# Optimization experiments

Hardware: AMD Instinct MI355X
Metric: run time of the kernel (lower is better)

## Reference

```python
import jax, jax.numpy as jnp
import numpy as np

OUT, IN = 14336, 4096          # Llama FFN up-projection
N = OUT * IN                   # total quantized elements
NB = N // 64                   # NF4 blocks (blocksize 64)
NG = N // 256                  # double-quant groups (group size 256)
B = 32                         # batch rows


def setup_inputs() -> dict:
    key = jax.random.key(0)
    ks = jax.random.split(key, 7)
    x = jax.random.normal(ks[0], (B, IN), dtype=jnp.float16)
    # packed bytes: two 4-bit nibbles per byte (values 0..255)
    packed = jax.random.randint(ks[1], (N // 2,), 0, 256, dtype=jnp.int32)
    absmax = jax.random.uniform(ks[2], (NB,), dtype=jnp.float32)                     # per-block absmax
    code = jax.random.uniform(ks[3], (NB,), jnp.float32, minval=0.5, maxval=1.5)     # per-block code scale
    offset = jax.random.uniform(ks[4], (NB,), jnp.float32, minval=0.0, maxval=8.0)   # per-block offset
    g_absmax = jax.random.uniform(ks[5], (NG,), jnp.float32, minval=0.5, maxval=1.5) # nested (state2) absmax
    g_code = jax.random.uniform(ks[6], (NG,), jnp.float32, minval=0.5, maxval=1.5)   # nested (state2) code
    return {"x": x, "packed": packed, "absmax": absmax, "code": code,
            "offset": offset, "g_absmax": g_absmax, "g_code": g_code}


def _dequantize_nf4(packed, absmax, code, offset, g_absmax, g_code):
    # Unpack nibbles: even element = low nibble (byte & 15), odd = high nibble (byte >> 4)
    low = packed & 15
    high = packed >> 4
    nib = jnp.stack([low, high], axis=-1).reshape(-1).astype(jnp.float32)  # [N]
    # Nested (double) dequantization scales, matching the Triton kernel:
    # combined_scale = (absmax / code) * (g_absmax / g_code)
    block_scale = absmax / code                      # [NB]
    group_scale = g_absmax / g_code                  # [NG]
    cs_block = block_scale * jnp.repeat(group_scale, 64 * 4 // 64)  # each group spans 4 blocks -> [NB]
    cs = jnp.repeat(cs_block, 64)                    # per-element combined scale [N]
    off = jnp.repeat(offset, 64)                     # per-element offset [N]
    # dequantized = nibble * cs - offset * cs (as written in the kernel), stored as fp16
    deq = (nib * cs - off * cs).astype(jnp.float16)
    return deq.reshape(OUT, IN)


def reference(x, packed, absmax, code, offset, g_absmax, g_code):
    W = _dequantize_nf4(packed, absmax, code, offset, g_absmax, g_code)  # [OUT, IN] fp16
    return x @ W.T                                                        # [B, OUT] fp16
```

## Files before the change

kernel.cpp:

```cpp
#include <hip/hip_runtime.h>
#include <hip/hip_bf16.h>


#define OUT_D 14336
#define IN_D  4096
#define B_D   32
#define KC    256
#define OTILE 32
#define CHUNKS (IN_D / KC)
#define LSTRIDE 264

typedef __attribute__((ext_vector_type(4))) float f32x4;
typedef __attribute__((ext_vector_type(4))) int   i32x4;
typedef __bf16 bf16x8 __attribute__((ext_vector_type(8)));
typedef __bf16 bf16x4 __attribute__((ext_vector_type(4)));
using u16 = unsigned short;

__global__ __launch_bounds__(256) void nf4_linear_kernel(
    const float* __restrict__ x,
    const int*  __restrict__ packed,
    const float* __restrict__ absmax,
    const float* __restrict__ code,
    const float* __restrict__ offset,
    const float* __restrict__ g_absmax,
    const float* __restrict__ g_code,
    float* __restrict__ out)
{
    __shared__ u16 wlds[2][OTILE * LSTRIDE];
    __shared__ u16 xlds[2][B_D * LSTRIDE];

    const int t      = threadIdx.x;
    const int o_base = blockIdx.x * OTILE;

    const int wrow = t >> 3;
    const int wseg = t & 7;
    const int o    = o_base + wrow;

    const int wave   = t >> 6;
    const int lane   = t & 63;
    const int m_base = (wave & 1) * 16;
    const int n_base = (wave >> 1) * 16;
    const int frow   = lane & 15;
    const int kk     = (lane >> 4) * 8;

    const int* pbase = packed + o * (IN_D / 2) + wseg * 16;

    f32x4 acc = {0.f, 0.f, 0.f, 0.f};

    i32x4 pkA[4], pkB[4];
    f32x4 pxA[8], pxB[8];
    float amA, cdA, ofA, gaA, gcA;
    float amB, cdB, ofB, gaB, gcB;

#define LOADPK(DST, KCI) { \
    const i32x4* ps = reinterpret_cast<const i32x4*>(pbase + (KCI) * (KC / 2)); \
    DST[0] = ps[0]; DST[1] = ps[1]; DST[2] = ps[2]; DST[3] = ps[3]; }

#define LOADPX(DST, KCI) { \
    const float* xb = x + (KCI) * KC; \
    _Pragma("unroll") \
    for (int j = 0; j < 8; ++j) { \
        int li = t + j * 256; \
        DST[j] = *reinterpret_cast<const f32x4*>(xb + (li >> 6) * IN_D + (li & 63) * 4); } }

#define LOADSC(AM, CD, OF, GA, GC, KCI) { \
    int bidx = o * 64 + (KCI) * 4 + (wseg >> 1); \
    int gidx = o * 16 + (KCI); \
    AM = absmax[bidx]; CD = code[bidx]; OF = offset[bidx]; \
    GA = g_absmax[gidx]; GC = g_code[gidx]; }

#define BODY(PK, PX, AM, CD, OF, GA, GC, PKN, PXN, AMN, CDN, OFN, GAN, GCN, KCI) { \
     \
    if ((KCI) + 1 < CHUNKS) { \
        LOADPK(PKN, (KCI) + 1); \
        LOADPX(PXN, (KCI) + 1); \
        LOADSC(AMN, CDN, OFN, GAN, GCN, (KCI) + 1); \
    } \
     \
    { \
        const float cs  = (AM / CD) * (GA / GC); \
        const float noc = -OF * cs; \
        u16* wdst = &wlds[p][wrow * LSTRIDE + wseg * 32]; \
        _Pragma("unroll") \
        for (int j = 0; j < 4; ++j) { \
            bf16x8 r; \
            _Pragma("unroll") \
            for (int wi = 0; wi < 4; ++wi) { \
                int w = PK[j][wi]; \
                r[wi * 2]     = (__bf16)fmaf((float)(w & 15),        cs, noc); \
                r[wi * 2 + 1] = (__bf16)fmaf((float)((w >> 4) & 15), cs, noc); \
            } \
            *reinterpret_cast<bf16x8*>(wdst + j * 8) = r; \
        } \
    } \
     \
    { \
        _Pragma("unroll") \
        for (int j = 0; j < 8; ++j) { \
            int li = t + j * 256; \
            bf16x4 h; \
            h[0] = (__bf16)PX[j][0]; h[1] = (__bf16)PX[j][1]; \
            h[2] = (__bf16)PX[j][2]; h[3] = (__bf16)PX[j][3]; \
            *reinterpret_cast<bf16x4*>(&xlds[p][(li >> 6) * LSTRIDE + (li & 63) * 4]) = h; \
        } \
    } \
    __syncthreads(); \
     \
    { \
        const u16* xp = &xlds[p][(m_base + frow) * LSTRIDE + kk]; \
        const u16* wp = &wlds[p][(n_base + frow) * LSTRIDE + kk]; \
        _Pragma("unroll") \
        for (int ks = 0; ks < KC / 32; ++ks) { \
            bf16x8 a = *reinterpret_cast<const bf16x8*>(xp + ks * 32); \
            bf16x8 b = *reinterpret_cast<const bf16x8*>(wp + ks * 32); \
            acc = __builtin_amdgcn_mfma_f32_16x16x32_bf16(a, b, acc, 0, 0, 0); \
        } \
    } \
    p ^= 1; }

    LOADPK(pkA, 0);
    LOADPX(pxA, 0);
    LOADSC(amA, cdA, ofA, gaA, gcA, 0);

    int p = 0;
    for (int ic = 0; ic < CHUNKS; ic += 2) {
        BODY(pkA, pxA, amA, cdA, ofA, gaA, gcA,
             pkB, pxB, amB, cdB, ofB, gaB, gcB, ic);
        BODY(pkB, pxB, amB, cdB, ofB, gaB, gcB,
             pkA, pxA, amA, cdA, ofA, gaA, gcA, ic + 1);
    }

    const int oc = o_base + n_base + frow;
    const int r0 = m_base + (lane >> 4) * 4;
    #pragma unroll
    for (int i = 0; i < 4; ++i) {
        out[(r0 + i) * OUT_D + oc] = acc[i];
    }
}

extern "C" void kernel_launch(void* const* d_in, const int* in_sizes, int n_in,
                              void* d_out, int out_size, void* d_ws, size_t ws_size,
                              hipStream_t stream) {
    const void* px = nullptr;
    const void* ppk = nullptr;
    const void* trio[3] = {nullptr, nullptr, nullptr};
    const void* pair[2] = {nullptr, nullptr};
    int ntrio = 0, npair = 0;
    const int SZ_X   = B_D * IN_D;
    const int SZ_PK  = OUT_D * (IN_D / 2);
    const int SZ_NB  = OUT_D * (IN_D / 64);
    const int SZ_NG  = OUT_D * (IN_D / 256);
    for (int i = 0; i < n_in; ++i) {
        int s = in_sizes[i];
        if (s == SZ_X) px = d_in[i];
        else if (s == SZ_PK) ppk = d_in[i];
        else if (s == SZ_NB) { if (ntrio < 3) trio[ntrio++] = d_in[i]; }
        else if (s == SZ_NG) { if (npair < 2) pair[npair++] = d_in[i]; }
    }
    if (!px || !ppk || ntrio != 3 || npair != 2) {
        px = d_in[0]; ppk = d_in[1];
        trio[0] = d_in[2]; trio[1] = d_in[3]; trio[2] = d_in[4];
        pair[0] = d_in[5]; pair[1] = d_in[6];
    }

    nf4_linear_kernel<<<dim3(OUT_D / OTILE), dim3(256), 0, stream>>>(
        (const float*)px, (const int*)ppk,
        (const float*)trio[0], (const float*)trio[1], (const float*)trio[2],
        (const float*)pair[0], (const float*)pair[1],
        (float*)d_out);
}
```

Measured before the change: 42.31 us.

## Split K across two blocks with atomic accumulation and smaller chunks

Adds a split-K dimension (KSPLIT=2) to the grid so each block handles half of the input dimension, halving chunk size to 128 and accumulating partial outputs with atomicAdd after a memset of the output. The 448-block grid becomes 896 blocks, which is meant to fill more of the GPU's compute units and hide memory latency. Per-block scales are now precomputed at load time, and launch bounds request 4 blocks per CU. The cost is an extra memset launch, atomic traffic on the output, and more loop iterations with barriers.

```diff
diff --git a/kernel.cpp b/kernel.cpp
--- a/kernel.cpp
+++ b/kernel.cpp
@@ -5,10 +5,11 @@
 #define OUT_D 14336
 #define IN_D  4096
 #define B_D   32
-#define KC    256
+#define KC    128
 #define OTILE 32
-#define CHUNKS (IN_D / KC)
-#define LSTRIDE 264
+#define KSPLIT 2
+#define CHUNKS (IN_D / KC / KSPLIT)
+#define LSTRIDE 136
 
 typedef __attribute__((ext_vector_type(4))) float f32x4;
 typedef __attribute__((ext_vector_type(4))) int   i32x4;
@@ -16,7 +17,7 @@
 typedef __bf16 bf16x4 __attribute__((ext_vector_type(4)));
 using u16 = unsigned short;
 
-__global__ __launch_bounds__(256) void nf4_linear_kernel(
+__global__ __launch_bounds__(256, 4) void nf4_kernel(
     const float* __restrict__ x,
     const int*  __restrict__ packed,
     const float* __restrict__ absmax,
@@ -31,6 +32,7 @@
 
     const int t      = threadIdx.x;
     const int o_base = blockIdx.x * OTILE;
+    const int kz     = blockIdx.y;
 
     const int wrow = t >> 3;
     const int wseg = t & 7;
@@ -43,69 +45,67 @@
     const int frow   = lane & 15;
     const int kk     = (lane >> 4) * 8;
 
-    const int* pbase = packed + o * (IN_D / 2) + wseg * 16;
+    const int*   pbase = packed + o * (IN_D / 2) + kz * (IN_D / 4);
+    const float* xbase = x + kz * (IN_D / 2);
+    const int    sb    = o * 64 + kz * 32;
+    const int    gb    = o * 16;
 
     f32x4 acc = {0.f, 0.f, 0.f, 0.f};
 
-    i32x4 pkA[4], pkB[4];
-    f32x4 pxA[8], pxB[8];
-    float amA, cdA, ofA, gaA, gcA;
-    float amB, cdB, ofB, gaB, gcB;
+    i32x4 pkA[2], pkB[2];
+    f32x4 pxA[4], pxB[4];
+    float csA[2], nocA[2], csB[2], nocB[2];
 
-#define LOADPK(DST, KCI) { \
-    const i32x4* ps = reinterpret_cast<const i32x4*>(pbase + (KCI) * (KC / 2)); \
-    DST[0] = ps[0]; DST[1] = ps[1]; DST[2] = ps[2]; DST[3] = ps[3]; }
+#define LOADPK(DST, C) { \
+    DST[0] = *reinterpret_cast<const i32x4*>(pbase + (C) * 64 + wseg * 4); \
+    DST[1] = *reinterpret_cast<const i32x4*>(pbase + (C) * 64 + 32 + wseg * 4); }
 
-#define LOADPX(DST, KCI) { \
-    const float* xb = x + (KCI) * KC; \
+#define LOADPX(DST, C) { \
     _Pragma("unroll") \
-    for (int j = 0; j < 8; ++j) { \
-        int li = t + j * 256; \
-        DST[j] = *reinterpret_cast<const f32x4*>(xb + (li >> 6) * IN_D + (li & 63) * 4); } }
+    for (int j2 = 0; j2 < 4; ++j2) { \
+        int li = t + j2 * 256; \
+        DST[j2] = *reinterpret_cast<const f32x4*>( \
+            xbase + (li >> 5) * IN_D + (C) * KC + (li & 31) * 4); } }
 
-#define LOADSC(AM, CD, OF, GA, GC, KCI) { \
-    int bidx = o * 64 + (KCI) * 4 + (wseg >> 1); \
-    int gidx = o * 16 + (KCI); \
-    AM = absmax[bidx]; CD = code[bidx]; OF = offset[bidx]; \
-    GA = g_absmax[gidx]; GC = g_code[gidx]; }
+#define LOADSC(CS, NOC, C) { \
+    _Pragma("unroll") \
+    for (int j = 0; j < 2; ++j) { \
+        int blk = kz * 32 + (C) * 2 + j;        \
+        int bi  = sb + (C) * 2 + j; \
+        int gi  = gb + (blk >> 2); \
+        float am = absmax[bi], cd = code[bi], of = offset[bi]; \
+        float ga = g_absmax[gi], gc = g_code[gi]; \
+        CS[j]  = (am * ga) / (cd * gc); \
+        NOC[j] = -of * CS[j]; } }
 
-#define BODY(PK, PX, AM, CD, OF, GA, GC, PKN, PXN, AMN, CDN, OFN, GAN, GCN, KCI) { \
-     \
-    if ((KCI) + 1 < CHUNKS) { \
-        LOADPK(PKN, (KCI) + 1); \
-        LOADPX(PXN, (KCI) + 1); \
-        LOADSC(AMN, CDN, OFN, GAN, GCN, (KCI) + 1); \
+#define BODY(PK, PX, CS, NOC, PKN, PXN, CSN, NOCN, C) { \
+    if ((C) + 1 < CHUNKS) { \
+        LOADPK(PKN, (C) + 1) \
+        LOADPX(PXN, (C) + 1) \
+        LOADSC(CSN, NOCN, (C) + 1) \
     } \
      \
-    { \
-        const float cs  = (AM / CD) * (GA / GC); \
-        const float noc = -OF * cs; \
-        u16* wdst = &wlds[p][wrow * LSTRIDE + wseg * 32]; \
+    _Pragma("unroll") \
+    for (int j = 0; j < 2; ++j) { \
+        bf16x8 r; \
         _Pragma("unroll") \
-        for (int j = 0; j < 4; ++j) { \
-            bf16x8 r; \
-            _Pragma("unroll") \
-            for (int wi = 0; wi < 4; ++wi) { \
-                int w = PK[j][wi]; \
-                r[wi * 2]     = (__bf16)fmaf((float)(w & 15),        cs, noc); \
-                r[wi * 2 + 1] = (__bf16)fmaf((float)((w >> 4) & 15), cs, noc); \
-            } \
-            *reinterpret_cast<bf16x8*>(wdst + j * 8) = r; \
+        for (int q = 0; q < 4; ++q) { \
+            int w = PK[j][q]; \
+            r[2 * q]     = (__bf16)fmaf((float)(w & 15),        CS[j], NOC[j]); \
+            r[2 * q + 1] = (__bf16)fmaf((float)((w >> 4) & 15), CS[j], NOC[j]); \
         } \
+        *reinterpret_cast<bf16x8*>(&wlds[p][wrow * LSTRIDE + (j * 8 + wseg) * 8]) = r; \
     } \
      \
-    { \
-        _Pragma("unroll") \
-        for (int j = 0; j < 8; ++j) { \
-            int li = t + j * 256; \
-            bf16x4 h; \
-            h[0] = (__bf16)PX[j][0]; h[1] = (__bf16)PX[j][1]; \
-            h[2] = (__bf16)PX[j][2]; h[3] = (__bf16)PX[j][3]; \
-            *reinterpret_cast<bf16x4*>(&xlds[p][(li >> 6) * LSTRIDE + (li & 63) * 4]) = h; \
-        } \
+    _Pragma("unroll") \
+    for (int j2 = 0; j2 < 4; ++j2) { \
+        int li = t + j2 * 256; \
+        bf16x4 h; \
+        h[0] = (__bf16)PX[j2][0]; h[1] = (__bf16)PX[j2][1]; \
+        h[2] = (__bf16)PX[j2][2]; h[3] = (__bf16)PX[j2][3]; \
+        *reinterpret_cast<bf16x4*>(&xlds[p][(li >> 5) * LSTRIDE + (li & 31) * 4]) = h; \
     } \
     __syncthreads(); \
-     \
     { \
         const u16* xp = &xlds[p][(m_base + frow) * LSTRIDE + kk]; \
         const u16* wp = &wlds[p][(n_base + frow) * LSTRIDE + kk]; \
@@ -118,24 +118,26 @@
     } \
     p ^= 1; }
 
-    LOADPK(pkA, 0);
-    LOADPX(pxA, 0);
-    LOADSC(amA, cdA, ofA, gaA, gcA, 0);
+    LOADPK(pkA, 0)
+    LOADPX(pxA, 0)
+    LOADSC(csA, nocA, 0)
 
     int p = 0;
     for (int ic = 0; ic < CHUNKS; ic += 2) {
-        BODY(pkA, pxA, amA, cdA, ofA, gaA, gcA,
-             pkB, pxB, amB, cdB, ofB, gaB, gcB, ic);
-        BODY(pkB, pxB, amB, cdB, ofB, gaB, gcB,
-             pkA, pxA, amA, cdA, ofA, gaA, gcA, ic + 1);
+        BODY(pkA, pxA, csA, nocA, pkB, pxB, csB, nocB, ic)
+        BODY(pkB, pxB, csB, nocB, pkA, pxA, csA, nocA, ic + 1)
     }
 
     const int oc = o_base + n_base + frow;
     const int r0 = m_base + (lane >> 4) * 4;
     #pragma unroll
     for (int i = 0; i < 4; ++i) {
-        out[(r0 + i) * OUT_D + oc] = acc[i];
+        atomicAdd(&out[(r0 + i) * OUT_D + oc], acc[i]);
     }
+#undef LOADPK
+#undef LOADPX
+#undef LOADSC
+#undef BODY
 }
 
 extern "C" void kernel_launch(void* const* d_in, const int* in_sizes, int n_in,
@@ -163,7 +165,9 @@
         pair[0] = d_in[5]; pair[1] = d_in[6];
     }
 
-    nf4_linear_kernel<<<dim3(OUT_D / OTILE), dim3(256), 0, stream>>>(
+    hipMemsetAsync(d_out, 0, (size_t)out_size * sizeof(float), stream);
+
+    nf4_kernel<<<dim3(OUT_D / OTILE, KSPLIT), dim3(256), 0, stream>>>(
         (const float*)px, (const int*)ppk,
         (const float*)trio[0], (const float*)trio[1], (const float*)trio[2],
         (const float*)pair[0], (const float*)pair[1],
```

Result: slower. 44.33 us (+4.8%).
